# Kernel tuning notes

Measured on AMD Instinct MI355X. Metric: run time of the kernel, lower is better.

The kernel has to match this reference:

```python
import jax, jax.numpy as jnp
import numpy as np

B, L, DIM = 2, 2048, 768
NH, HD = 12, 64  # num_heads, head_dim; NH*HD == dim_attn == 768


def setup_inputs() -> dict:
    key = jax.random.key(0)
    ks = jax.random.split(key, 7)
    x = jax.random.normal(ks[0], (B, L, DIM), dtype=jnp.float32)
    pos_bias = jax.random.normal(ks[1], (1, NH, L, L), dtype=jnp.float32)
    Wq = jax.random.normal(ks[2], (DIM, DIM), dtype=jnp.float32) * 0.02
    Wk = jax.random.normal(ks[3], (DIM, DIM), dtype=jnp.float32) * 0.02
    Wv = jax.random.normal(ks[4], (DIM, DIM), dtype=jnp.float32) * 0.02
    Wo = jax.random.normal(ks[5], (DIM, DIM), dtype=jnp.float32) * 0.02
    mask = jax.random.randint(ks[6], (B, L), 0, 2, dtype=jnp.int32)
    return {"x": x, "pos_bias": pos_bias, "Wq": Wq, "Wk": Wk, "Wv": Wv,
            "Wo": Wo, "mask": mask}


def reference(x, pos_bias, Wq, Wk, Wv, Wo, mask):
    b, l, _ = x.shape
    # q/k/v projections (torch Linear: x @ W.T), split into heads
    q = (x @ Wq.T).reshape(b, l, NH, HD)
    k = (x @ Wk.T).reshape(b, l, NH, HD)
    v = (x @ Wv.T).reshape(b, l, NH, HD)
    # additive bias [B, H, Lq, Lk]: pos_bias broadcast + key mask -> -inf
    neg_inf = jnp.finfo(x.dtype).min
    attn_bias = jnp.broadcast_to(pos_bias, (b, NH, l, l))
    attn_bias = jnp.where(mask[:, None, None, :] == 0, neg_inf, attn_bias)
    # T5-style attention: NO 1/sqrt(d) scaling
    scores = jnp.einsum('binc,bjnc->bnij', q, k) + attn_bias
    attn = jax.nn.softmax(scores.astype(jnp.float32), axis=-1).astype(x.dtype)
    out = jnp.einsum('bnij,bjnc->binc', attn, v).reshape(b, l, NH * HD)
    return out @ Wo.T
```

## Files before the change

kernel.cpp:

```cpp
#include <hip/hip_runtime.h>
#include <math.h>

#define Bq 2
#define Lq 2048
#define DIMq 768
#define NHq 12
#define HDq 64
#define LOG2E 1.44269504f

typedef __attribute__((ext_vector_type(8))) short short8;
typedef __attribute__((ext_vector_type(4))) short short4v;
typedef __attribute__((ext_vector_type(4))) float float4v;

typedef __attribute__((address_space(3))) unsigned int as3_u32;
typedef __attribute__((address_space(1))) unsigned int as1_u32;

static __device__ __forceinline__ short f2bf(float f) {
    union { float f; unsigned u; } v; v.f = f;
    unsigned r = (v.u + 0x7FFF + ((v.u >> 16) & 1)) >> 16;
    return (short)r;
}

static __device__ __forceinline__ void gld_lds16(const short* g, short* l) {
    __builtin_amdgcn_global_load_lds((const as1_u32*)g, (as3_u32*)l, 16, 0, 0);
}

__global__ __launch_bounds__(256)
void to_bf16(const float* __restrict__ x,  const float* __restrict__ wq,
             const float* __restrict__ wk, const float* __restrict__ wv,
             const float* __restrict__ wo,
             short* __restrict__ xb, short* __restrict__ wqb,
             short* __restrict__ wkb, short* __restrict__ wvb,
             short* __restrict__ wob)
{
    int blk = blockIdx.x;
    const float* s; short* d; int off;
    if      (blk <  768) { s = x;  d = xb;  off = blk * 1024; }
    else if (blk <  912) { s = wq; d = wqb; off = (blk -  768) * 1024; }
    else if (blk < 1056) { s = wk; d = wkb; off = (blk -  912) * 1024; }
    else if (blk < 1200) { s = wv; d = wvb; off = (blk - 1056) * 1024; }
    else                 { s = wo; d = wob; off = (blk - 1200) * 1024; }
    const float4* s4 = (const float4*)s;
    short4v* d4 = (short4v*)d;
#pragma unroll
    for (int i = 0; i < 4; ++i) {
        int idx = off + threadIdx.x + i * 256;
        float4 v = s4[idx];
        short4v o;
        o[0] = f2bf(v.x); o[1] = f2bf(v.y); o[2] = f2bf(v.z); o[3] = f2bf(v.w);
        d4[idx] = o;
    }
}

template<int BN>
__global__ __launch_bounds__(256, 3)
void gemm_bf16(const short* __restrict__ A,
               const short* __restrict__ W0, const short* __restrict__ W1,
               const short* __restrict__ W2,
               short* __restrict__ D0, short* __restrict__ D1,
               short* __restrict__ D2, float* __restrict__ DF, int mode)
{
    constexpr int NT = BN / 32;
    const int z = blockIdx.z;
    const short* W = (z == 0) ? W0 : ((z == 1) ? W1 : W2);
    short* DH = (z == 0) ? D0 : ((z == 1) ? D1 : D2);

    __shared__ __align__(16) short As[128][64];
    __shared__ __align__(16) short Ws[BN][64];

    const int tid  = threadIdx.x;
    const int wave = tid >> 6;
    const int lane = tid & 63;
    const int col  = lane & 15;
    const int quad = lane >> 4;
    const int wr = wave >> 1, wc = wave & 1;
    const int m0 = blockIdx.y * 128, n0 = blockIdx.x * BN;

    float4v acc[4][NT];
#pragma unroll
    for (int mt = 0; mt < 4; ++mt)
#pragma unroll
        for (int nt = 0; nt < NT; ++nt) acc[mt][nt] = (float4v){0.f, 0.f, 0.f, 0.f};

    const short* Ab = A + (size_t)m0 * DIMq;
    const short* Wb = W + (size_t)n0 * DIMq;

    for (int k0 = 0; k0 < DIMq; k0 += 64) {
        __syncthreads();
#pragma unroll
        for (int i = 0; i < 4; ++i) {
            int g = i * 256 + tid;
            int row = g >> 3, ch = g & 7;
            gld_lds16(Ab + (size_t)row * DIMq + k0 + ch * 8, (short*)As + g * 8);
        }
#pragma unroll
        for (int i = 0; i < BN / 32; ++i) {
            int g = i * 256 + tid;
            int row = g >> 3, ch = g & 7;
            gld_lds16(Wb + (size_t)row * DIMq + k0 + ch * 8, (short*)Ws + g * 8);
        }
        __syncthreads();
#pragma unroll
        for (int kk = 0; kk < 2; ++kk) {
            short8 a[4], bfr[NT];
#pragma unroll
            for (int mt = 0; mt < 4; ++mt)
                a[mt] = *(const short8*)&As[wr * 64 + mt * 16 + col][kk * 32 + quad * 8];
#pragma unroll
            for (int nt = 0; nt < NT; ++nt)
                bfr[nt] = *(const short8*)&Ws[wc * (BN / 2) + nt * 16 + col][kk * 32 + quad * 8];
#pragma unroll
            for (int mt = 0; mt < 4; ++mt)
#pragma unroll
                for (int nt = 0; nt < NT; ++nt)
                    acc[mt][nt] = __builtin_amdgcn_mfma_f32_16x16x32_bf16(
                        a[mt], bfr[nt], acc[mt][nt], 0, 0, 0);
        }
    }

#pragma unroll
    for (int mt = 0; mt < 4; ++mt)
#pragma unroll
    for (int reg = 0; reg < 4; ++reg) {
        int m = m0 + wr * 64 + mt * 16 + quad * 4 + reg;
#pragma unroll
        for (int nt = 0; nt < NT; ++nt) {
            int n = n0 + wc * (BN / 2) + nt * 16 + col;
            if (mode == 1) {
                int b = m >> 11, l = m & 2047, h = n >> 6, c = n & 63;
                DH[(((size_t)(b * NHq + h)) * Lq + l) * HDq + c] = f2bf(acc[mt][nt][reg]);
            } else {
                DF[(size_t)m * DIMq + n] = acc[mt][nt][reg];
            }
        }
    }
}

__global__ __launch_bounds__(256)
void transpose_v(const short* __restrict__ Vh, short* __restrict__ VT)
{
    const int lt = blockIdx.x;
    const int bh = blockIdx.y;
    const short* src = Vh + ((size_t)bh * Lq + lt * 64) * HDq;
    short* dst = VT + (size_t)bh * HDq * Lq + lt * 64;
    __shared__ __align__(16) short t[64][72];
    const int tid = threadIdx.x;
    {
        int row = tid & 63, seg = tid >> 6;
        *(short8*)&t[row][seg * 16]     = *(const short8*)&src[row * HDq + seg * 16];
        *(short8*)&t[row][seg * 16 + 8] = *(const short8*)&src[row * HDq + seg * 16 + 8];
    }
    __syncthreads();
    {
        int c = tid >> 2, seg = tid & 3;
        short8 o0, o1;
#pragma unroll
        for (int j = 0; j < 8; ++j) o0[j] = t[seg * 16 + j][c];
#pragma unroll
        for (int j = 0; j < 8; ++j) o1[j] = t[seg * 16 + 8 + j][c];
        *(short8*)&dst[(size_t)c * Lq + seg * 16]     = o0;
        *(short8*)&dst[(size_t)c * Lq + seg * 16 + 8] = o1;
    }
}

__global__ __launch_bounds__(512, 6)
void attn_fwd_mfma(const short* __restrict__ Qh, const short* __restrict__ Kh,
                   const short* __restrict__ VT, const float* __restrict__ pos_bias,
                   const int* __restrict__ mask, short* __restrict__ AO)
{
    const int hw = blockIdx.x;
    const int logical = (hw & 7) * 96 + (hw >> 3);
    const int b  = logical & 1;
    const int qt = (logical >> 1) & 31;
    const int h  = logical >> 6;

    const short* Q = Qh + ((size_t)(b * NHq + h)) * Lq * HDq;
    const short* K = Kh + ((size_t)(b * NHq + h)) * Lq * HDq;
    const short* V = VT + ((size_t)(b * NHq + h)) * HDq * Lq;
    const int* mk = mask + (size_t)b * Lq;

    __shared__ __align__(16) short Ks[2][64][72];
    __shared__ __align__(16) short Vt[2][64][72];
    __shared__ __align__(16) short Ps[64][72];
    __shared__ float lbuf[8][16];

    const int tid  = threadIdx.x;
    const int wave = tid >> 6;
    const int lane = tid & 63;
    const int col  = lane & 15;
    const int quad = lane >> 4;
    const int wrow = wave >> 1;
    const int wkey = wave & 1;

    short8 qa[2];
    {
        const short* qrow = Q + (size_t)(qt * 64 + wrow * 16 + col) * HDq;
        qa[0] = *(const short8*)&qrow[quad * 8];
        qa[1] = *(const short8*)&qrow[32 + quad * 8];
    }

    const float* brow = pos_bias + (size_t)h * Lq * Lq
                      + (size_t)(qt * 64 + wrow * 16 + quad * 4) * Lq + col;

    float bcur[2][4], bnxt[2][4];
    auto prefetch = [&](int kt, float (&bb)[2][4]) {
#pragma unroll
        for (int ntl = 0; ntl < 2; ++ntl) {
            int nt = wkey * 2 + ntl;
            int mval = mk[kt * 64 + nt * 16 + col];
            float fm = (mval == 0) ? -1e30f : 0.0f;
#pragma unroll
            for (int reg = 0; reg < 4; ++reg)
                bb[ntl][reg] = (brow[(size_t)reg * Lq + kt * 64 + nt * 16] + fm) * LOG2E;
        }
    };

    short8 kreg, vreg;
    auto loadKV = [&](int kt) {
        int row = tid >> 3, ch = tid & 7;
        kreg = *(const short8*)&K[(size_t)(kt * 64 + row) * HDq + ch * 8];
        vreg = *(const short8*)&V[(size_t)row * Lq + kt * 64 + ch * 8];
    };
    auto writeKV = [&](int buf) {
        int row = tid >> 3, ch = tid & 7;
        *(short8*)&Ks[buf][row][ch * 8] = kreg;
        *(short8*)&Vt[buf][row][ch * 8] = vreg;
    };

    float4v Oacc[2];
    float l_part[4];
#pragma unroll
    for (int ntl = 0; ntl < 2; ++ntl) Oacc[ntl] = (float4v){0.f, 0.f, 0.f, 0.f};
#pragma unroll
    for (int r = 0; r < 4; ++r) l_part[r] = 0.f;

    loadKV(0);
    writeKV(0);
    prefetch(0, bcur);
    __syncthreads();

    int cur = 0;
    for (int kt = 0; kt < Lq / 64; ++kt) {
        const bool more = (kt + 1 < Lq / 64);
        if (more) {
            loadKV(kt + 1);
            prefetch(kt + 1, bnxt);
        }

        float4v S[2];
#pragma unroll
        for (int ntl = 0; ntl < 2; ++ntl) S[ntl] = (float4v){0.f, 0.f, 0.f, 0.f};
        __builtin_amdgcn_s_setprio(1);
#pragma unroll
        for (int kk = 0; kk < 2; ++kk) {
#pragma unroll
            for (int ntl = 0; ntl < 2; ++ntl) {
                short8 bfr = *(const short8*)
                    &Ks[cur][(wkey * 2 + ntl) * 16 + col][kk * 32 + quad * 8];
                S[ntl] = __builtin_amdgcn_mfma_f32_16x16x32_bf16(qa[kk], bfr, S[ntl], 0, 0, 0);
            }
        }
        __builtin_amdgcn_s_setprio(0);

#pragma unroll
        for (int ntl = 0; ntl < 2; ++ntl)
#pragma unroll
            for (int reg = 0; reg < 4; ++reg) {
                float p = __builtin_amdgcn_exp2f(
                    __builtin_fmaf(S[ntl][reg], LOG2E, bcur[ntl][reg]));
                l_part[reg] += p;
                Ps[wrow * 16 + quad * 4 + reg][(wkey * 2 + ntl) * 16 + col] = f2bf(p);
            }
        __syncthreads();

        __builtin_amdgcn_s_setprio(1);
#pragma unroll
        for (int kk = 0; kk < 2; ++kk) {
            short8 pa = *(const short8*)&Ps[wrow * 16 + col][kk * 32 + quad * 8];
#pragma unroll
            for (int ntl = 0; ntl < 2; ++ntl) {
                short8 vb = *(const short8*)
                    &Vt[cur][(wkey * 2 + ntl) * 16 + col][kk * 32 + quad * 8];
                Oacc[ntl] = __builtin_amdgcn_mfma_f32_16x16x32_bf16(pa, vb, Oacc[ntl], 0, 0, 0);
            }
        }
        __builtin_amdgcn_s_setprio(0);

        if (more) writeKV(cur ^ 1);
        __syncthreads();
        cur ^= 1;

#pragma unroll
        for (int ntl = 0; ntl < 2; ++ntl)
#pragma unroll
            for (int reg = 0; reg < 4; ++reg)
                bcur[ntl][reg] = bnxt[ntl][reg];
    }

    float lown[4];
#pragma unroll
    for (int reg = 0; reg < 4; ++reg) {
        float v = l_part[reg];
#pragma unroll
        for (int off = 1; off < 16; off <<= 1)
            v += __shfl_xor(v, off, 64);
        lown[reg] = v;
    }
    if (col == 0) {
#pragma unroll
        for (int reg = 0; reg < 4; ++reg)
            lbuf[wave][quad * 4 + reg] = lown[reg];
    }
    __syncthreads();

    short* aorow = AO + ((size_t)b * Lq + qt * 64 + wrow * 16 + quad * 4) * DIMq
                 + h * HDq + wkey * 32 + col;
#pragma unroll
    for (int reg = 0; reg < 4; ++reg) {
        float inv = 1.0f / (lown[reg] + lbuf[wave ^ 1][quad * 4 + reg]);
#pragma unroll
        for (int ntl = 0; ntl < 2; ++ntl)
            aorow[(size_t)reg * DIMq + 16 * ntl] = f2bf(Oacc[ntl][reg] * inv);
    }
}

extern "C" void kernel_launch(void* const* d_in, const int* in_sizes, int n_in,
                              void* d_out, int out_size, void* d_ws, size_t ws_size,
                              hipStream_t stream) {
    const float* x        = (const float*)d_in[0];
    const float* pos_bias = (const float*)d_in[1];
    const float* Wq       = (const float*)d_in[2];
    const float* Wk       = (const float*)d_in[3];
    const float* Wv       = (const float*)d_in[4];
    const float* Wo       = (const float*)d_in[5];
    const int*   mask     = (const int*)d_in[6];
    float* out = (float*)d_out;

    const size_t nX = (size_t)Bq * Lq * DIMq;
    const size_t nW = (size_t)DIMq * DIMq;
    short* xb  = (short*)d_ws;
    short* wqb = xb  + nX;
    short* wkb = wqb + nW;
    short* wvb = wkb + nW;
    short* wob = wvb + nW;
    short* Qh  = wob + nW;
    short* Kh  = Qh  + nX;
    short* Vh  = Kh  + nX;
    short* AOb = Vh  + nX;
    short* VTb = xb;

    dim3 blk(256);
    hipLaunchKernelGGL(to_bf16, dim3(1344), blk, 0, stream,
                       x, Wq, Wk, Wv, Wo, xb, wqb, wkb, wvb, wob);

    hipLaunchKernelGGL((gemm_bf16<128>), dim3(DIMq / 128, (Bq * Lq) / 128, 3), blk, 0, stream,
                       xb, wqb, wkb, wvb, Qh, Kh, Vh, (float*)nullptr, 1);

    hipLaunchKernelGGL(transpose_v, dim3(Lq / 64, Bq * NHq), blk, 0, stream,
                       Vh, VTb);

    hipLaunchKernelGGL(attn_fwd_mfma, dim3(Lq / 64 * NHq * Bq), dim3(512), 0, stream,
                       Qh, Kh, VTb, pos_bias, mask, AOb);

    hipLaunchKernelGGL((gemm_bf16<64>), dim3(DIMq / 64, (Bq * Lq) / 128, 1), blk, 0, stream,
                       AOb, wob, wob, wob, (short*)nullptr, (short*)nullptr,
                       (short*)nullptr, out, 0);
}
```

Before: 382.4 us.

## Restructure attention kernel to register-resident P with per-wave key split and LDS reduction

```diff
diff --git a/kernel.cpp b/kernel.cpp
--- a/kernel.cpp
+++ b/kernel.cpp
@@ -11,6 +11,7 @@
 typedef __attribute__((ext_vector_type(8))) short short8;
 typedef __attribute__((ext_vector_type(4))) short short4v;
 typedef __attribute__((ext_vector_type(4))) float float4v;
+typedef __attribute__((ext_vector_type(4))) int int4v;
 
 typedef __attribute__((address_space(3))) unsigned int as3_u32;
 typedef __attribute__((address_space(1))) unsigned int as1_u32;
@@ -20,6 +21,18 @@
     unsigned r = (v.u + 0x7FFF + ((v.u >> 16) & 1)) >> 16;
     return (short)r;
 }
+
+#if __has_builtin(__builtin_amdgcn_mfma_f32_16x16x16bf16_1k)
+static __device__ __forceinline__ float4v mfma16(short4v a, short4v b, float4v c) {
+    return __builtin_amdgcn_mfma_f32_16x16x16bf16_1k(a, b, c, 0, 0, 0);
+}
+#else
+static __device__ __forceinline__ float4v mfma16(short4v a, short4v b, float4v c) {
+    asm volatile("s_nop 1\n\tv_mfma_f32_16x16x16_bf16 %0, %1, %2, %0"
+                 : "+v"(c) : "v"(a), "v"(b));
+    return c;
+}
+#endif
 
 static __device__ __forceinline__ void gld_lds16(const short* g, short* l) {
     __builtin_amdgcn_global_load_lds((const as1_u32*)g, (as3_u32*)l, 16, 0, 0);
@@ -163,7 +176,7 @@
     }
 }
 
-__global__ __launch_bounds__(512, 6)
+__global__ __launch_bounds__(512, 4)
 void attn_fwd_mfma(const short* __restrict__ Qh, const short* __restrict__ Kh,
                    const short* __restrict__ VT, const float* __restrict__ pos_bias,
                    const int* __restrict__ mask, short* __restrict__ AO)
@@ -179,148 +192,140 @@
     const short* V = VT + ((size_t)(b * NHq + h)) * HDq * Lq;
     const int* mk = mask + (size_t)b * Lq;
 
-    __shared__ __align__(16) short Ks[2][64][72];
-    __shared__ __align__(16) short Vt[2][64][72];
-    __shared__ __align__(16) short Ps[64][72];
-    __shared__ float lbuf[8][16];
+    __shared__ float Ored[2][64][33];
+    __shared__ float lbuf[2][4][2][16];
 
     const int tid  = threadIdx.x;
     const int wave = tid >> 6;
     const int lane = tid & 63;
     const int col  = lane & 15;
     const int quad = lane >> 4;
-    const int wrow = wave >> 1;
-    const int wkey = wave & 1;
-
-    short8 qa[2];
+    const int qh = wave >> 2;
+    const int kg = wave & 3;
+
+    short8 qb[2][2];
+#pragma unroll
+    for (int mt = 0; mt < 2; ++mt) {
+        const short* qrow = Q + (size_t)(qt * 64 + qh * 32 + mt * 16 + col) * HDq;
+        qb[mt][0] = *(const short8*)&qrow[quad * 8];
+        qb[mt][1] = *(const short8*)&qrow[32 + quad * 8];
+    }
+
+    const float* bq = pos_bias + (size_t)h * Lq * Lq
+                    + (size_t)(qt * 64 + qh * 32 + col) * Lq + kg * 16 + quad * 4;
+
+    float4v bcur[2], bnxt[2];
+    auto prefetch = [&](int kt, float4v (&bb)[2]) {
+        int4v mv = *(const int4v*)&mk[kt * 64 + kg * 16 + quad * 4];
+        float4v fm;
+#pragma unroll
+        for (int j = 0; j < 4; ++j) fm[j] = (mv[j] == 0) ? -1e30f : 0.0f;
+#pragma unroll
+        for (int mt = 0; mt < 2; ++mt) {
+            float4v bv = *(const float4v*)(bq + (size_t)mt * 16 * Lq + kt * 64);
+            bb[mt] = (bv + fm) * LOG2E;
+        }
+    };
+
+    float4v Oacc[2][4];
+    float l_part[2] = {0.f, 0.f};
+#pragma unroll
+    for (int mt = 0; mt < 2; ++mt)
+#pragma unroll
+        for (int dblk = 0; dblk < 4; ++dblk) Oacc[mt][dblk] = (float4v){0.f, 0.f, 0.f, 0.f};
+
+    prefetch(0, bcur);
+
+    for (int kt = 0; kt < Lq / 64; ++kt) {
+        if (kt + 1 < Lq / 64) prefetch(kt + 1, bnxt);
+
+        const short* krow = K + (size_t)(kt * 64 + kg * 16 + col) * HDq;
+        short8 ka0 = *(const short8*)&krow[quad * 8];
+        short8 ka1 = *(const short8*)&krow[32 + quad * 8];
+
+        float4v St[2] = {(float4v){0.f, 0.f, 0.f, 0.f}, (float4v){0.f, 0.f, 0.f, 0.f}};
+        __builtin_amdgcn_s_setprio(1);
+        St[0] = __builtin_amdgcn_mfma_f32_16x16x32_bf16(ka0, qb[0][0], St[0], 0, 0, 0);
+        St[1] = __builtin_amdgcn_mfma_f32_16x16x32_bf16(ka0, qb[1][0], St[1], 0, 0, 0);
+        St[0] = __builtin_amdgcn_mfma_f32_16x16x32_bf16(ka1, qb[0][1], St[0], 0, 0, 0);
+        St[1] = __builtin_amdgcn_mfma_f32_16x16x32_bf16(ka1, qb[1][1], St[1], 0, 0, 0);
+        __builtin_amdgcn_s_setprio(0);
+
+        short4v pb[2];
+#pragma unroll
+        for (int mt = 0; mt < 2; ++mt) {
+            float s0 = 0.f;
+#pragma unroll
+            for (int j = 0; j < 4; ++j) {
+                float p = __builtin_amdgcn_exp2f(
+                    __builtin_fmaf(St[mt][j], LOG2E, bcur[mt][j]));
+                s0 += p;
+                pb[mt][j] = f2bf(p);
+            }
+            l_part[mt] += s0;
+        }
+
+        __builtin_amdgcn_s_setprio(1);
+#pragma unroll
+        for (int dblk = 0; dblk < 4; ++dblk) {
+            short4v va = *(const short4v*)
+                &V[(size_t)(dblk * 16 + col) * Lq + kt * 64 + kg * 16 + quad * 4];
+            Oacc[0][dblk] = mfma16(va, pb[0], Oacc[0][dblk]);
+            Oacc[1][dblk] = mfma16(va, pb[1], Oacc[1][dblk]);
+        }
+        __builtin_amdgcn_s_setprio(0);
+
+        bcur[0] = bnxt[0];
+        bcur[1] = bnxt[1];
+    }
+
+#pragma unroll
+    for (int mt = 0; mt < 2; ++mt) {
+        float v = l_part[mt];
+        v += __shfl_xor(v, 16, 64);
+        v += __shfl_xor(v, 32, 64);
+        l_part[mt] = v;
+    }
+    if (quad == 0) {
+#pragma unroll
+        for (int mt = 0; mt < 2; ++mt)
+            lbuf[qh][kg][mt][col] = l_part[mt];
+    }
+
+#pragma unroll
+    for (int r = 0; r < 4; ++r) {
+        if (r > 0) __syncthreads();
+        if (kg == r) {
+#pragma unroll
+            for (int mt = 0; mt < 2; ++mt)
+#pragma unroll
+                for (int dblk = 0; dblk < 4; ++dblk)
+#pragma unroll
+                    for (int reg = 0; reg < 4; ++reg) {
+                        int d = dblk * 16 + quad * 4 + reg;
+                        int q = mt * 16 + col;
+                        if (r == 0) Ored[qh][d][q]  = Oacc[mt][dblk][reg];
+                        else        Ored[qh][d][q] += Oacc[mt][dblk][reg];
+                    }
+        }
+    }
+    __syncthreads();
+
     {
-        const short* qrow = Q + (size_t)(qt * 64 + wrow * 16 + col) * HDq;
-        qa[0] = *(const short8*)&qrow[quad * 8];
-        qa[1] = *(const short8*)&qrow[32 + quad * 8];
-    }
-
-    const float* brow = pos_bias + (size_t)h * Lq * Lq
-                      + (size_t)(qt * 64 + wrow * 16 + quad * 4) * Lq + col;
-
-    float bcur[2][4], bnxt[2][4];
-    auto prefetch = [&](int kt, float (&bb)[2][4]) {
-#pragma unroll
-        for (int ntl = 0; ntl < 2; ++ntl) {
-            int nt = wkey * 2 + ntl;
-            int mval = mk[kt * 64 + nt * 16 + col];
-            float fm = (mval == 0) ? -1e30f : 0.0f;
-#pragma unroll
-            for (int reg = 0; reg < 4; ++reg)
-                bb[ntl][reg] = (brow[(size_t)reg * Lq + kt * 64 + nt * 16] + fm) * LOG2E;
-        }
-    };
-
-    short8 kreg, vreg;
-    auto loadKV = [&](int kt) {
-        int row = tid >> 3, ch = tid & 7;
-        kreg = *(const short8*)&K[(size_t)(kt * 64 + row) * HDq + ch * 8];
-        vreg = *(const short8*)&V[(size_t)row * Lq + kt * 64 + ch * 8];
-    };
-    auto writeKV = [&](int buf) {
-        int row = tid >> 3, ch = tid & 7;
-        *(short8*)&Ks[buf][row][ch * 8] = kreg;
-        *(short8*)&Vt[buf][row][ch * 8] = vreg;
-    };
-
-    float4v Oacc[2];
-    float l_part[4];
-#pragma unroll
-    for (int ntl = 0; ntl < 2; ++ntl) Oacc[ntl] = (float4v){0.f, 0.f, 0.f, 0.f};
-#pragma unroll
-    for (int r = 0; r < 4; ++r) l_part[r] = 0.f;
-
-    loadKV(0);
-    writeKV(0);
-    prefetch(0, bcur);
-    __syncthreads();
-
-    int cur = 0;
-    for (int kt = 0; kt < Lq / 64; ++kt) {
-        const bool more = (kt + 1 < Lq / 64);
-        if (more) {
-            loadKV(kt + 1);
-            prefetch(kt + 1, bnxt);
-        }
-
-        float4v S[2];
-#pragma unroll
-        for (int ntl = 0; ntl < 2; ++ntl) S[ntl] = (float4v){0.f, 0.f, 0.f, 0.f};
-        __builtin_amdgcn_s_setprio(1);
-#pragma unroll
-        for (int kk = 0; kk < 2; ++kk) {
-#pragma unroll
-            for (int ntl = 0; ntl < 2; ++ntl) {
-                short8 bfr = *(const short8*)
-                    &Ks[cur][(wkey * 2 + ntl) * 16 + col][kk * 32 + quad * 8];
-                S[ntl] = __builtin_amdgcn_mfma_f32_16x16x32_bf16(qa[kk], bfr, S[ntl], 0, 0, 0);
-            }
-        }
-        __builtin_amdgcn_s_setprio(0);
-
-#pragma unroll
-        for (int ntl = 0; ntl < 2; ++ntl)
-#pragma unroll
-            for (int reg = 0; reg < 4; ++reg) {
-                float p = __builtin_amdgcn_exp2f(
-                    __builtin_fmaf(S[ntl][reg], LOG2E, bcur[ntl][reg]));
-                l_part[reg] += p;
-                Ps[wrow * 16 + quad * 4 + reg][(wkey * 2 + ntl) * 16 + col] = f2bf(p);
-            }
-        __syncthreads();
-
-        __builtin_amdgcn_s_setprio(1);
-#pragma unroll
-        for (int kk = 0; kk < 2; ++kk) {
-            short8 pa = *(const short8*)&Ps[wrow * 16 + col][kk * 32 + quad * 8];
-#pragma unroll
-            for (int ntl = 0; ntl < 2; ++ntl) {
-                short8 vb = *(const short8*)
-                    &Vt[cur][(wkey * 2 + ntl) * 16 + col][kk * 32 + quad * 8];
-                Oacc[ntl] = __builtin_amdgcn_mfma_f32_16x16x32_bf16(pa, vb, Oacc[ntl], 0, 0, 0);
-            }
-        }
-        __builtin_amdgcn_s_setprio(0);
-
-        if (more) writeKV(cur ^ 1);
-        __syncthreads();
-        cur ^= 1;
-
-#pragma unroll
-        for (int ntl = 0; ntl < 2; ++ntl)
-#pragma unroll
-            for (int reg = 0; reg < 4; ++reg)
-                bcur[ntl][reg] = bnxt[ntl][reg];
-    }
-
-    float lown[4];
-#pragma unroll
-    for (int reg = 0; reg < 4; ++reg) {
-        float v = l_part[reg];
-#pragma unroll
-        for (int off = 1; off < 16; off <<= 1)
-            v += __shfl_xor(v, off, 64);
-        lown[reg] = v;
-    }
-    if (col == 0) {
-#pragma unroll
-        for (int reg = 0; reg < 4; ++reg)
-            lbuf[wave][quad * 4 + reg] = lown[reg];
-    }
-    __syncthreads();
-
-    short* aorow = AO + ((size_t)b * Lq + qt * 64 + wrow * 16 + quad * 4) * DIMq
-                 + h * HDq + wkey * 32 + col;
-#pragma unroll
-    for (int reg = 0; reg < 4; ++reg) {
-        float inv = 1.0f / (lown[reg] + lbuf[wave ^ 1][quad * 4 + reg]);
-#pragma unroll
-        for (int ntl = 0; ntl < 2; ++ntl)
-            aorow[(size_t)reg * DIMq + 16 * ntl] = f2bf(Oacc[ntl][reg] * inv);
+        const int qh_t = tid >> 8;
+        const int tt = tid & 255;
+        const int q  = tt >> 3;
+        const int d0 = (tt & 7) * 8;
+        const int mtq = q >> 4, qc = q & 15;
+        float l = lbuf[qh_t][0][mtq][qc] + lbuf[qh_t][1][mtq][qc]
+                + lbuf[qh_t][2][mtq][qc] + lbuf[qh_t][3][mtq][qc];
+        float inv = 1.0f / l;
+        short8 o;
+#pragma unroll
+        for (int j = 0; j < 8; ++j)
+            o[j] = f2bf(Ored[qh_t][d0 + j][q] * inv);
+        *(short8*)&AO[((size_t)b * Lq + qt * 64 + qh_t * 32 + q) * DIMq
+                      + h * HDq + d0] = o;
     }
 }
 
```

Result: slower. 482.4 us (+26.2%).
